# Kernel optimization log

Hardware: AMD Instinct MI355X
Metric: run time of the kernel (lower is better)

## Reference

```python
import jax, jax.numpy as jnp
import numpy as np
from jax import lax

T = 64      # timesteps == number of stacked LSTM layers (per source)
B = 128     # lstm_batchsize (hardcoded)
H = 64      # BasicLSTMCell(64)


def _cell(x_in, c, h, W, b):
    # TF BasicLSTMCell, forget_bias=0.0, gate order: i, j, f, o
    z = jnp.concatenate([x_in, h], axis=-1) @ W + b          # [B, 4H]
    i, j, f, o = jnp.split(z, 4, axis=-1)
    c2 = c * jax.nn.sigmoid(f) + jax.nn.sigmoid(i) * jnp.tanh(j)
    h2 = jnp.tanh(c2) * jax.nn.sigmoid(o)
    return c2, h2


def setup_inputs() -> dict:
    key = jax.random.key(0)
    ks = jax.random.split(key, 8)
    s = 0.1
    x = jax.random.normal(ks[0], (B, T, 1), dtype=jnp.float32)
    labels = jax.random.normal(ks[1], (B, T, 1), dtype=jnp.float32)
    # layer 0: input dim 1; layers 1..T-1: input dim H
    W0 = jax.random.normal(ks[2], (1 + H, 4 * H), dtype=jnp.float32) * s
    b0 = jnp.zeros((4 * H,), dtype=jnp.float32)
    Wl = jax.random.normal(ks[3], (T - 1, H + H, 4 * H), dtype=jnp.float32) * s
    bl = jnp.zeros((T - 1, 4 * H), dtype=jnp.float32)
    # time_distributed fully_connected(1, relu): separate weights per timestep
    Wd = jax.random.normal(ks[4], (T, H, 1), dtype=jnp.float32) * s
    bd = jnp.zeros((T, 1), dtype=jnp.float32)
    return {"x": x, "labels": labels, "W0": W0, "b0": b0,
            "Wl": Wl, "bl": bl, "Wd": Wd, "bd": bd}


def reference(x, labels, W0, b0, Wl, bl, Wd, bd):
    def step(carry, x_t):
        cs, hs = carry                      # each [T, B, H]
        c0, h0 = _cell(x_t, cs[0], hs[0], W0, b0)

        def layer_step(h_in, lp):
            c, h_prev, W, b = lp
            c2, h2 = _cell(h_in, c, h_prev, W, b)
            return h2, (c2, h2)

        h_top, (cs_r, hs_r) = lax.scan(layer_step, h0, (cs[1:], hs[1:], Wl, bl))
        new_cs = jnp.concatenate([c0[None], cs_r], axis=0)
        new_hs = jnp.concatenate([h0[None], hs_r], axis=0)
        return (new_cs, new_hs), h_top

    init = (jnp.zeros((T, B, H), x.dtype), jnp.zeros((T, B, H), x.dtype))
    xs = jnp.transpose(x, (1, 0, 2))        # [T, B, 1]
    _, outs = lax.scan(step, init, xs)      # outs: [T, B, H]
    outs = jnp.transpose(outs, (1, 0, 2))   # [B, T, H]

    # per-timestep dense + relu
    pred = jax.nn.relu(jnp.einsum('bth,tho->bto', outs, Wd) + bd[None])  # [B, T, 1]
    loss = jnp.mean(jnp.square(labels - pred))
    return pred, loss
```

## Files before the change

### kernel.cpp

```cpp
#include <hip/hip_runtime.h>
#include <hip/hip_bf16.h>
#include <hip/hip_fp8.h>

#define TT 64
#define LL 64
#define BB 128
#define HH 64
#define GG 4
#define NG 16
#define SL 8
#define RR 16
#define SB (TT + GG - 1)

typedef short v8s __attribute__((ext_vector_type(8)));
typedef float v4f __attribute__((ext_vector_type(4)));


__device__ __forceinline__ float sigm(float z)   {
    return __builtin_amdgcn_rcpf(1.f + __expf(-z));
}
__device__ __forceinline__ float tanh_f(float z) {
    return fmaf(-2.f, __builtin_amdgcn_rcpf(1.f + __expf(2.f * z)), 1.f);
}

__device__ __forceinline__ void prefetch8(const unsigned long long* fast,
                                          const unsigned long long* ins,
                                          unsigned long long* f, unsigned long long* i) {
    asm volatile(
        "global_load_dwordx2 %0, %8, off sc0\n\t"
        "global_load_dwordx2 %1, %8, off offset:8 sc0\n\t"
        "global_load_dwordx2 %2, %8, off offset:64 sc0\n\t"
        "global_load_dwordx2 %3, %8, off offset:72 sc0\n\t"
        "global_load_dwordx2 %4, %9, off sc0 sc1\n\t"
        "global_load_dwordx2 %5, %9, off offset:8 sc0 sc1\n\t"
        "global_load_dwordx2 %6, %9, off offset:64 sc0 sc1\n\t"
        "global_load_dwordx2 %7, %9, off offset:72 sc0 sc1"
        : "=v"(f[0]), "=v"(f[1]), "=v"(f[2]), "=v"(f[3]),
          "=v"(i[0]), "=v"(i[1]), "=v"(i[2]), "=v"(i[3])
        : "v"(fast), "v"(ins)
        : "memory");
}
__device__ __forceinline__ void waitv(unsigned long long* f, unsigned long long* i) {
    asm volatile("s_waitcnt vmcnt(0)"
                 : "+v"(f[0]), "+v"(f[1]), "+v"(f[2]), "+v"(f[3]),
                   "+v"(i[0]), "+v"(i[1]), "+v"(i[2]), "+v"(i[3])
                 :: "memory");
}
__device__ __forceinline__ void gstore64_dual(unsigned long long* pf,
                                              unsigned long long* pi,
                                              unsigned long long v) {
    asm volatile(
        "global_store_dwordx2 %0, %2, off\n\t"
        "global_store_dwordx2 %1, %2, off sc0 sc1"
        :: "v"(pf), "v"(pi), "v"(v) : "memory");
}
__device__ __forceinline__ int fload(const int* p) {
    int v;
    asm volatile("global_load_dword %0, %1, off sc0 sc1\n\ts_waitcnt vmcnt(0)"
                 : "=v"(v) : "v"(p) : "memory");
    return v;
}
__device__ __forceinline__ void fstore(int* p, int v) {
    asm volatile("global_store_dword %0, %1, off sc0 sc1"
                 :: "v"(p), "v"(v) : "memory");
}
__device__ __forceinline__ void barrier_lds() {
    asm volatile("s_waitcnt lgkmcnt(0)\n\ts_barrier" ::: "memory");
}
__device__ __forceinline__ unsigned short f2bf(float f) {
    unsigned u = __float_as_uint(f);
    return (unsigned short)((u + 0x8000u) >> 16);
}

__global__ __launch_bounds__(512, 2) void lstm_pipeline(
    const float* __restrict__ x,
    const float* __restrict__ W0,
    const float* __restrict__ b0,
    const float* __restrict__ Wl,
    const float* __restrict__ bl,
    int* __restrict__ prog,
    unsigned long long* __restrict__ hglobI,
    unsigned long long* __restrict__ hglobF,
    float* __restrict__ htop)
{
    const int g   = blockIdx.x >> 3;
    const int s   = blockIdx.x & 7;
    const int tid = threadIdx.x;
    const int wv  = tid >> 6;
    const int k   = wv >> 1;
    const int nh  = wv & 1;
    const int ln  = tid & 63;
    const int lr  = ln & 15;
    const int qd  = ln >> 4;
    const int l   = GG * g + k;

    __shared__ unsigned short hL[GG][2][RR * 72];
    __shared__ float xbuf[RR * 65];

    if (blockIdx.x == 0 && tid < 2) fstore(&prog[300 + tid], 0);

    for (int i = tid; i < GG * 2 * RR * 72; i += 512)
        ((unsigned short*)hL)[i] = 0;
    if (g == 0) {
        for (int i = tid; i < RR * 64; i += 512)
            xbuf[(i >> 6) * 65 + (i & 63)] =
                x[(size_t)(s * RR + (i >> 6)) * TT + (i & 63)];
    }

    v8s bfr[32];
#pragma unroll
    for (int f = 0; f < 32; ++f) {
        const int kf = f & 3, tn = f >> 2;
        const int ga = tn & 3, ut = tn >> 2;
        const int gc = ga * 64 + nh * 32 + ut * 16 + lr;
        v8s tmp;
#pragma unroll
        for (int j = 0; j < 8; ++j) {
            const int kk = kf * 32 + qd * 8 + j;
            float v;
            if (l > 0)        v = Wl[((size_t)(l - 1) * 128 + kk) * 256 + gc];
            else if (kk == 0) v = W0[gc];
            else if (kk < 64) v = 0.f;
            else              v = W0[(size_t)(kk - 63) * 256 + gc];
            tmp[j] = (short)f2bf(v);
        }
        bfr[f] = tmp;
    }

    const float* bs = l ? (bl + (l - 1) * 256) : b0;
    float bias[8];
#pragma unroll
    for (int i = 0; i < 8; ++i) {
        const int ut = i >> 2, ga = i & 3;
        bias[i] = bs[ga * 64 + nh * 32 + ut * 16 + lr];
    }

    float cst[8];
#pragma unroll
    for (int i = 0; i < 8; ++i) cst[i] = 0.f;

    unsigned long long pfF[4], pfI[4];
    const bool poller = (k == 0) && (g > 0);
#define TAGOFF(T) (((((size_t)((T) & 15) * NG + (g - 1)) * SL + s) * RR + lr) * 16 + qd * 2)
    if (poller)
        prefetch8(hglobF + TAGOFF(0), hglobI + TAGOFF(0), pfF, pfI);

    __syncthreads();

    for (int sb = 0; sb < SB; ++sb) {
        const int t = sb - k;
        const bool active = (t >= 0) && (t < TT);
        const int rd = (sb - 1) & 1, wr = sb & 1;

        if (active) {
            const int row = lr * 72;
            v8s a2 = *(const v8s*)&hL[k][rd][row + qd * 8];
            v8s a3 = *(const v8s*)&hL[k][rd][row + 32 + qd * 8];
            v8s a0, a1;
            if (k > 0) {
                a0 = *(const v8s*)&hL[k - 1][rd][row + qd * 8];
                a1 = *(const v8s*)&hL[k - 1][rd][row + 32 + qd * 8];
            } else if (g > 0) {
                waitv(pfF, pfI);
                unsigned int okF = 1, okI = 1;
#pragma unroll
                for (int q2 = 0; q2 < 4; ++q2) {
                    okF &= (unsigned int)((unsigned int)(pfF[q2] >> 32) == (unsigned int)t);
                    okI &= (unsigned int)((unsigned int)(pfI[q2] >> 32) == (unsigned int)t);
                }
                unsigned int bw0, bw1, bw2, bw3;
                if (okF | okI) {
                    const unsigned long long* pick = okF ? pfF : pfI;
                    bw0 = (unsigned int)pick[0]; bw1 = (unsigned int)pick[1];
                    bw2 = (unsigned int)pick[2]; bw3 = (unsigned int)pick[3];
                } else {
                    for (;;) {
                        prefetch8(hglobF + TAGOFF(t), hglobI + TAGOFF(t), pfF, pfI);
                        waitv(pfF, pfI);
                        unsigned int oF = 1, oI = 1;
#pragma unroll
                        for (int q2 = 0; q2 < 4; ++q2) {
                            oF &= (unsigned int)((unsigned int)(pfF[q2] >> 32) == (unsigned int)t);
                            oI &= (unsigned int)((unsigned int)(pfI[q2] >> 32) == (unsigned int)t);
                        }
                        if (oF | oI) {
                            const unsigned long long* pick = oF ? pfF : pfI;
                            bw0 = (unsigned int)pick[0]; bw1 = (unsigned int)pick[1];
                            bw2 = (unsigned int)pick[2]; bw3 = (unsigned int)pick[3];
                            break;
                        }
                    }
                }
                if (nh == 0 && ln == 0) fstore(&prog[s * NG + g], t + 1);
                if (t + 1 < TT)
                    prefetch8(hglobF + TAGOFF(t + 1), hglobI + TAGOFF(t + 1), pfF, pfI);
                unsigned int ws4[4] = {bw0, bw1, bw2, bw3};
#pragma unroll
                for (int wi = 0; wi < 2; ++wi)
#pragma unroll
                    for (int bi = 0; bi < 4; ++bi) {
                        __hip_fp8_e4m3 f8;
                        f8.__x = (ws4[wi] >> (8 * bi)) & 0xff;
                        a0[wi * 4 + bi] = (short)f2bf((float)f8);
                        f8.__x = (ws4[2 + wi] >> (8 * bi)) & 0xff;
                        a1[wi * 4 + bi] = (short)f2bf((float)f8);
                    }
            } else {
                a0 = (v8s){0, 0, 0, 0, 0, 0, 0, 0};
                a1 = (v8s){0, 0, 0, 0, 0, 0, 0, 0};
                if (qd == 0) a0[0] = (short)f2bf(xbuf[lr * 65 + t]);
            }

            v4f acc[8];
#pragma unroll
            for (int i = 0; i < 8; ++i) acc[i] = (v4f){0.f, 0.f, 0.f, 0.f};
#pragma unroll
            for (int tn = 0; tn < 8; ++tn) {
                v4f c = acc[tn];
                c = __builtin_amdgcn_mfma_f32_16x16x32_bf16(a2, bfr[tn * 4 + 2], c, 0, 0, 0);
                c = __builtin_amdgcn_mfma_f32_16x16x32_bf16(a3, bfr[tn * 4 + 3], c, 0, 0, 0);
                c = __builtin_amdgcn_mfma_f32_16x16x32_bf16(a0, bfr[tn * 4 + 0], c, 0, 0, 0);
                c = __builtin_amdgcn_mfma_f32_16x16x32_bf16(a1, bfr[tn * 4 + 1], c, 0, 0, 0);
                acc[tn] = c;
            }

            if (k == 3 && g < NG - 1 && t >= 16 && (t & 7) == 0)
                while (fload(&prog[s * NG + (g + 1)]) < t - 7) {}

            const size_t dbase = (((size_t)(t & 15) * NG + g) * SL + s) * RR * 16;
#pragma unroll
            for (int ut = 0; ut < 2; ++ut) {
                const int u = nh * 32 + ut * 16 + lr;
#pragma unroll
                for (int r = 0; r < 4; ++r) {
                    float zi = acc[ut * 4 + 0][r] + bias[ut * 4 + 0];
                    float zj = acc[ut * 4 + 1][r] + bias[ut * 4 + 1];
                    float zf = acc[ut * 4 + 2][r] + bias[ut * 4 + 2];
                    float zo = acc[ut * 4 + 3][r] + bias[ut * 4 + 3];
                    float c2 = cst[ut * 4 + r] * sigm(zf) + sigm(zi) * tanh_f(zj);
                    cst[ut * 4 + r] = c2;
                    float h2 = tanh_f(c2) * sigm(zo);
                    const int b = qd * 4 + r;
                    hL[k][wr][b * 72 + u] = f2bf(h2);
                    if (k == 3) {
                        if (g < NG - 1) {
                            __hip_fp8_e4m3 f8(h2);
                            unsigned int pk = ((unsigned int)f8.__x) << (8 * (lr & 3));
                            pk |= __shfl_xor(pk, 1);
                            pk |= __shfl_xor(pk, 2);
                            if ((lr & 3) == 0) {
                                const size_t o = dbase + (size_t)b * 16 + nh * 8 + ut * 4 + (lr >> 2);
                                gstore64_dual(hglobF + o, hglobI + o,
                                              (unsigned long long)pk |
                                              ((unsigned long long)(unsigned int)t << 32));
                            }
                        } else {
                            htop[((size_t)t * HH + u) * BB + s * RR + b] = h2;
                        }
                    }
                }
            }
        }
        barrier_lds();
    }
}

__global__ __launch_bounds__(128, 1) void epilogue(
    const float* __restrict__ htop, const float* __restrict__ Wd,
    const float* __restrict__ bd, const float* __restrict__ labels,
    float* __restrict__ out, int* __restrict__ prog)
{
    int t = blockIdx.x, b = threadIdx.x;
    float s = 0.f;
#pragma unroll 4
    for (int h = 0; h < HH; ++h)
        s = fmaf(htop[(size_t)t * HH * BB + h * BB + b], Wd[t * HH + h], s);
    s += bd[t];
    s = fmaxf(s, 0.f);
    out[b * TT + t] = s;
    float d = labels[b * TT + t] - s;
    float e = d * d;
#pragma unroll
    for (int off = 32; off > 0; off >>= 1) e += __shfl_down(e, off, 64);
    __shared__ float ws2[2];
    if ((b & 63) == 0) ws2[b >> 6] = e;
    __syncthreads();
    if (b == 0) {
        float* loss = (float*)&prog[300];
        atomicAdd(loss, ws2[0] + ws2[1]);
        __builtin_amdgcn_s_waitcnt(0);
        int done = __hip_atomic_fetch_add(&prog[301], 1, __ATOMIC_ACQ_REL,
                                          __HIP_MEMORY_SCOPE_AGENT);
        if (done == 63) {
            float tot = __hip_atomic_load(loss, __ATOMIC_RELAXED,
                                          __HIP_MEMORY_SCOPE_AGENT);
            out[BB * TT] = tot * (1.f / (BB * TT));
        }
    }
}

extern "C" void kernel_launch(void* const* d_in, const int* in_sizes, int n_in,
                              void* d_out, int out_size, void* d_ws, size_t ws_size,
                              hipStream_t stream) {
    const float* x      = (const float*)d_in[0];
    const float* labels = (const float*)d_in[1];
    const float* W0     = (const float*)d_in[2];
    const float* b0     = (const float*)d_in[3];
    const float* Wl     = (const float*)d_in[4];
    const float* bl     = (const float*)d_in[5];
    const float* Wd     = (const float*)d_in[6];
    const float* bd     = (const float*)d_in[7];
    float* out = (float*)d_out;

    char* base = (char*)d_ws;
    int*                prog   = (int*)base;
    unsigned long long* hglobI = (unsigned long long*)(base + 16384);
    unsigned long long* hglobF = (unsigned long long*)(base + 16384 + 4194304);
    float*              htop   = (float*)(base + 16384 + 8388608);

    lstm_pipeline<<<NG * SL, 512, 0, stream>>>(x, W0, b0, Wl, bl, prog,
                                               hglobI, hglobF, htop);
    epilogue<<<64, 128, 0, stream>>>(htop, Wd, bd, labels, out, prog);
}
```

Measured before the change: 509.4 us.

## Replace block barriers with LDS flag handshakes and drop cross-block backpressure

Removes the per-superstep s_barrier and replaces it with per-wave LDS ready/read flags, using a 4-deep h ring buffer so waves of adjacent layers can run ahead without full-workgroup sync. The global handoff buffer is indexed by full timestep instead of mod 16, which removes the downstream-progress backpressure polling and the progress stores, at the cost of a larger workspace. A short sleep is added to the inter-block spin loop to reduce polling pressure. Spin-waiting on relaxed LDS atomics adds risk of ordering or livelock issues.

```diff
diff --git a/kernel.cpp b/kernel.cpp
--- a/kernel.cpp
+++ b/kernel.cpp
@@ -21,6 +21,16 @@
 }
 __device__ __forceinline__ float tanh_f(float z) {
     return fmaf(-2.f, __builtin_amdgcn_rcpf(1.f + __expf(2.f * z)), 1.f);
+}
+
+__device__ __forceinline__ int ldsf(const int* p) {
+    return __hip_atomic_load(p, __ATOMIC_RELAXED, __HIP_MEMORY_SCOPE_WORKGROUP);
+}
+__device__ __forceinline__ void ldsw(int* p, int v) {
+    __hip_atomic_store(p, v, __ATOMIC_RELAXED, __HIP_MEMORY_SCOPE_WORKGROUP);
+}
+__device__ __forceinline__ void lgkm0() {
+    asm volatile("s_waitcnt lgkmcnt(0)" ::: "memory");
 }
 
 __device__ __forceinline__ void prefetch8(const unsigned long long* fast,
@@ -54,18 +64,9 @@
         "global_store_dwordx2 %1, %2, off sc0 sc1"
         :: "v"(pf), "v"(pi), "v"(v) : "memory");
 }
-__device__ __forceinline__ int fload(const int* p) {
-    int v;
-    asm volatile("global_load_dword %0, %1, off sc0 sc1\n\ts_waitcnt vmcnt(0)"
-                 : "=v"(v) : "v"(p) : "memory");
-    return v;
-}
 __device__ __forceinline__ void fstore(int* p, int v) {
     asm volatile("global_store_dword %0, %1, off sc0 sc1"
                  :: "v"(p), "v"(v) : "memory");
-}
-__device__ __forceinline__ void barrier_lds() {
-    asm volatile("s_waitcnt lgkmcnt(0)\n\ts_barrier" ::: "memory");
 }
 __device__ __forceinline__ unsigned short f2bf(float f) {
     unsigned u = __float_as_uint(f);
@@ -94,12 +95,16 @@
     const int qd  = ln >> 4;
     const int l   = GG * g + k;
 
-    __shared__ unsigned short hL[GG][2][RR * 72];
+    __shared__ unsigned short hL[GG][4][RR * 72];
     __shared__ float xbuf[RR * 65];
+    __shared__ int wf[GG][2];
+    __shared__ int rf[GG][2];
 
     if (blockIdx.x == 0 && tid < 2) fstore(&prog[300 + tid], 0);
-
-    for (int i = tid; i < GG * 2 * RR * 72; i += 512)
+    if (tid < 8)             ((int*)wf)[tid] = -1;
+    if (tid >= 8 && tid < 16) ((int*)rf)[tid - 8] = -1;
+
+    for (int i = tid; i < GG * 4 * RR * 72; i += 512)
         ((unsigned short*)hL)[i] = 0;
     if (g == 0) {
         for (int i = tid; i < RR * 64; i += 512)
@@ -141,7 +146,7 @@
 
     unsigned long long pfF[4], pfI[4];
     const bool poller = (k == 0) && (g > 0);
-#define TAGOFF(T) (((((size_t)((T) & 15) * NG + (g - 1)) * SL + s) * RR + lr) * 16 + qd * 2)
+#define TAGOFF(T) (((((size_t)(T) * NG + (g - 1)) * SL + s) * RR + lr) * 16 + qd * 2)
     if (poller)
         prefetch8(hglobF + TAGOFF(0), hglobI + TAGOFF(0), pfF, pfI);
 
@@ -150,16 +155,24 @@
     for (int sb = 0; sb < SB; ++sb) {
         const int t = sb - k;
         const bool active = (t >= 0) && (t < TT);
-        const int rd = (sb - 1) & 1, wr = sb & 1;
+        const int rb = (sb + 3) & 3, wb = sb & 3;
 
         if (active) {
+            const int need = sb - 1;
+            for (;;) {
+                int ok = (ldsf(&wf[k][0]) >= need) & (ldsf(&wf[k][1]) >= need);
+                if (k > 0)
+                    ok &= (ldsf(&wf[k - 1][0]) >= need) & (ldsf(&wf[k - 1][1]) >= need);
+                if (ok) break;
+            }
+
             const int row = lr * 72;
-            v8s a2 = *(const v8s*)&hL[k][rd][row + qd * 8];
-            v8s a3 = *(const v8s*)&hL[k][rd][row + 32 + qd * 8];
+            v8s a2 = *(const v8s*)&hL[k][rb][row + qd * 8];
+            v8s a3 = *(const v8s*)&hL[k][rb][row + 32 + qd * 8];
             v8s a0, a1;
             if (k > 0) {
-                a0 = *(const v8s*)&hL[k - 1][rd][row + qd * 8];
-                a1 = *(const v8s*)&hL[k - 1][rd][row + 32 + qd * 8];
+                a0 = *(const v8s*)&hL[k - 1][rb][row + qd * 8];
+                a1 = *(const v8s*)&hL[k - 1][rb][row + 32 + qd * 8];
             } else if (g > 0) {
                 waitv(pfF, pfI);
                 unsigned int okF = 1, okI = 1;
@@ -174,7 +187,7 @@
                     bw0 = (unsigned int)pick[0]; bw1 = (unsigned int)pick[1];
                     bw2 = (unsigned int)pick[2]; bw3 = (unsigned int)pick[3];
                 } else {
-                    for (;;) {
+                    for (int it = 0;; ++it) {
                         prefetch8(hglobF + TAGOFF(t), hglobI + TAGOFF(t), pfF, pfI);
                         waitv(pfF, pfI);
                         unsigned int oF = 1, oI = 1;
@@ -189,9 +202,9 @@
                             bw2 = (unsigned int)pick[2]; bw3 = (unsigned int)pick[3];
                             break;
                         }
+                        if (it > 2) __builtin_amdgcn_s_sleep(1);
                     }
                 }
-                if (nh == 0 && ln == 0) fstore(&prog[s * NG + g], t + 1);
                 if (t + 1 < TT)
                     prefetch8(hglobF + TAGOFF(t + 1), hglobI + TAGOFF(t + 1), pfF, pfI);
                 unsigned int ws4[4] = {bw0, bw1, bw2, bw3};
@@ -210,6 +223,8 @@
                 a1 = (v8s){0, 0, 0, 0, 0, 0, 0, 0};
                 if (qd == 0) a0[0] = (short)f2bf(xbuf[lr * 65 + t]);
             }
+            lgkm0();
+            if (ln == 0) ldsw(&rf[k][nh], sb);
 
             v4f acc[8];
 #pragma unroll
@@ -224,10 +239,15 @@
                 acc[tn] = c;
             }
 
-            if (k == 3 && g < NG - 1 && t >= 16 && (t & 7) == 0)
-                while (fload(&prog[s * NG + (g + 1)]) < t - 7) {}
-
-            const size_t dbase = (((size_t)(t & 15) * NG + g) * SL + s) * RR * 16;
+            const int need2 = sb - 3;
+            for (;;) {
+                int ok = (ldsf(&rf[k][0]) >= need2) & (ldsf(&rf[k][1]) >= need2);
+                if (k < GG - 1)
+                    ok &= (ldsf(&rf[k + 1][0]) >= need2) & (ldsf(&rf[k + 1][1]) >= need2);
+                if (ok) break;
+            }
+
+            const size_t dbase = (((size_t)t * NG + g) * SL + s) * RR * 16;
 #pragma unroll
             for (int ut = 0; ut < 2; ++ut) {
                 const int u = nh * 32 + ut * 16 + lr;
@@ -241,8 +261,8 @@
                     cst[ut * 4 + r] = c2;
                     float h2 = tanh_f(c2) * sigm(zo);
                     const int b = qd * 4 + r;
-                    hL[k][wr][b * 72 + u] = f2bf(h2);
-                    if (k == 3) {
+                    hL[k][wb][b * 72 + u] = f2bf(h2);
+                    if (k == GG - 1) {
                         if (g < NG - 1) {
                             __hip_fp8_e4m3 f8(h2);
                             unsigned int pk = ((unsigned int)f8.__x) << (8 * (lr & 3));
@@ -260,8 +280,11 @@
                     }
                 }
             }
+            lgkm0();
+            if (ln == 0) ldsw(&wf[k][nh], sb);
+        } else {
+            if (ln == 0) { ldsw(&rf[k][nh], sb); ldsw(&wf[k][nh], sb); }
         }
-        barrier_lds();
     }
 }
 
@@ -315,8 +338,8 @@
     char* base = (char*)d_ws;
     int*                prog   = (int*)base;
     unsigned long long* hglobI = (unsigned long long*)(base + 16384);
-    unsigned long long* hglobF = (unsigned long long*)(base + 16384 + 4194304);
-    float*              htop   = (float*)(base + 16384 + 8388608);
+    unsigned long long* hglobF = (unsigned long long*)(base + 16384 + 16777216);
+    float*              htop   = (float*)(base + 16384 + 33554432);
 
     lstm_pipeline<<<NG * SL, 512, 0, stream>>>(x, W0, b0, Wl, bl, prog,
                                                hglobI, hglobF, htop);
```

Result: faster. 490.9 us (-3.6%).
